# Optimization experiments

Hardware: AMD Instinct MI355X
Metric: run time of the kernel (lower is better)

## Reference

```python
import jax, jax.numpy as jnp
import numpy as np

B, L, F, DM, H, DFF, NL, PRED = 8, 1000, 7, 512, 8, 2048, 4, 50
DK = DM // H           # head dim 64
P = DK // 4            # learned-mask proj dim 16
EPS = 1e-5
SCALE = 1.0 / float(np.sqrt(DK))


def _ln(x, g, b):
    m = jnp.mean(x, -1, keepdims=True)
    v = jnp.mean((x - m) ** 2, -1, keepdims=True)
    return (x - m) / jnp.sqrt(v + EPS) * g + b


def _make_pe():
    pos = np.arange(L, dtype=np.float32)[:, None]
    div = np.exp(np.arange(0, DM, 2, dtype=np.float32) * (-np.log(10000.0) / DM))
    pe = np.zeros((L, DM), dtype=np.float32)
    pe[:, 0::2] = np.sin(pos * div)
    pe[:, 1::2] = np.cos(pos * div)
    return jnp.asarray(pe)


def setup_inputs() -> dict:
    key = jax.random.key(0)
    ks = iter(jax.random.split(key, 40))
    def w(shape, s=0.02):
        return jax.random.normal(next(ks), shape, jnp.float32) * s
    return {
        "x": jax.random.normal(next(ks), (B, L, F), jnp.float32),
        "emb_w": w((F, DM)), "emb_b": jnp.zeros((DM,), jnp.float32),
        "pe": _make_pe(),
        "Wq": w((NL, DM, DM)), "bq": jnp.zeros((NL, DM), jnp.float32),
        "Wk": w((NL, DM, DM)), "bk": jnp.zeros((NL, DM), jnp.float32),
        "Wv": w((NL, DM, DM)), "bv": jnp.zeros((NL, DM), jnp.float32),
        "Wo": w((NL, DM, DM)), "bo": jnp.zeros((NL, DM), jnp.float32),
        "W1": w((NL, DM, DFF)), "b1": jnp.zeros((NL, DFF), jnp.float32),
        "W2": w((NL, DFF, DM)), "b2": jnp.zeros((NL, DM), jnp.float32),
        "g1": jnp.ones((NL, DM), jnp.float32), "be1": jnp.zeros((NL, DM), jnp.float32),
        "g2": jnp.ones((NL, DM), jnp.float32), "be2": jnp.zeros((NL, DM), jnp.float32),
        "lm_qw": w((DK, P)), "lm_qb": jnp.zeros((P,), jnp.float32),
        "lm_kw": w((DK, P)), "lm_kb": jnp.zeros((P,), jnp.float32),
        "gn": jnp.ones((DM,), jnp.float32), "bn": jnp.zeros((DM,), jnp.float32),
        "fc_w": w((DM, PRED)), "fc_b": jnp.zeros((PRED,), jnp.float32),
    }


def reference(x, emb_w, emb_b, pe, Wq, bq, Wk, bk, Wv, bv, Wo, bo,
              W1, b1, W2, b2, g1, be1, g2, be2,
              lm_qw, lm_qb, lm_kw, lm_kb, gn, bn, fc_w, fc_b):
    # eval mode: dropout = identity
    h = x @ emb_w + emb_b + pe[None]                 # [B,L,DM]
    for i in range(NL):
        q = (h @ Wq[i] + bq[i]).reshape(B, L, H, DK)
        k = (h @ Wk[i] + bk[i]).reshape(B, L, H, DK)
        v = (h @ Wv[i] + bv[i]).reshape(B, L, H, DK)
        scores = jnp.einsum('blhd,bshd->bhls', q, k) * SCALE
        # shared LearnedMask: per-head Q/K projection to P dims, tanh bias
        qp = q @ lm_qw + lm_qb                       # [B,L,H,P]
        kp = k @ lm_kw + lm_kb                       # [B,S,H,P]
        scores = scores + jnp.tanh(jnp.einsum('blhp,bshp->bhls', qp, kp))
        attn = jax.nn.softmax(scores, axis=-1)       # mask_flag=False: no mask
        ctx = jnp.einsum('bhls,bshd->blhd', attn, v).reshape(B, L, DM)
        h = _ln(h + ctx @ Wo[i] + bo[i], g1[i], be1[i])
        y = jax.nn.relu(h @ W1[i] + b1[i]) @ W2[i] + b2[i]
        h2 = _ln(h + y, g2[i], be2[i])
        h = _ln(h2 + y, g2[i], be2[i])               # module applies norm2 twice
    h = _ln(h, gn, bn)                               # Encoder final norm
    return h[:, -1, :] @ fc_w + fc_b                 # [B, PRED]
```

## Files before the change

kernel.cpp:

```cpp
#include <hip/hip_runtime.h>
#include <math.h>

#define B_    8
#define L_    1000
#define F_    7
#define DM_   512
#define H_    8
#define DFF_  2048
#define NL_   4
#define PRED_ 50
#define DK_   64
#define P_    16
#define EPS_  1e-5f
#define QKVS  1792

#define L2E_   1.4426950408889634f
#define C_QS   0.18033688011112042f
#define BS_QP  2.8853900817779268f
#define SHFT_  24.0f

typedef unsigned short u16;
typedef __bf16 bf16x8 __attribute__((ext_vector_type(8)));
typedef float  f32x4  __attribute__((ext_vector_type(4)));

__device__ inline float wave_reduce_sum(float x) {
#pragma unroll
  for (int off = 32; off >= 1; off >>= 1) x += __shfl_xor(x, off, 64);
  return x;
}
__device__ inline u16 f2bf(float f) {
  unsigned int u = __float_as_uint(f);
  unsigned int r = u + 0x7FFFu + ((u >> 16) & 1u);
  return (u16)(r >> 16);
}
__device__ inline unsigned int pack2(float a, float b) {
  return (unsigned int)f2bf(a) | ((unsigned int)f2bf(b) << 16);
}
__device__ inline float bf2f(u16 u) { return __uint_as_float(((unsigned int)u) << 16); }
__device__ inline float fexp2(float x) { return __builtin_amdgcn_exp2f(x); }
__device__ inline float frcp(float x) { return __builtin_amdgcn_rcpf(x); }

union bfrag { bf16x8 b; uint4 q; u16 u[8]; };

__device__ inline void gload16(const u16* g, u16* l) {
  __builtin_amdgcn_global_load_lds(
      (const __attribute__((address_space(1))) void*)g,
      (__attribute__((address_space(3))) void*)l, 16, 0, 0);
}

__global__ __launch_bounds__(256)
void transpose_w(const float* __restrict__ in, u16* __restrict__ out,
                 int K, int N, size_t in_lstride, size_t out_lstride,
                 int row_off, int out_ld) {
  __shared__ float tile[32][33];
  int z = blockIdx.z;
  int kk0 = blockIdx.y * 32, nn0 = blockIdx.x * 32;
  int tx = threadIdx.x & 31, ty = threadIdx.x >> 5;
  const float* ip = in + z * in_lstride;
  u16* op = out + z * out_lstride;
#pragma unroll
  for (int i = 0; i < 4; i++)
    tile[ty + i * 8][tx] = ip[(size_t)(kk0 + ty + i * 8) * N + nn0 + tx];
  __syncthreads();
#pragma unroll
  for (int i = 0; i < 4; i++)
    op[(size_t)(row_off + nn0 + ty + i * 8) * out_ld + kk0 + tx] = f2bf(tile[tx][ty + i * 8]);
}

__global__ __launch_bounds__(256)
void wfuse_kernel(const float* __restrict__ Wq, const float* __restrict__ Wk,
                  const float* __restrict__ lmqw, const float* __restrict__ lmkw,
                  u16* __restrict__ Wt) {
  int hh = blockIdx.x, side = blockIdx.y, layer = blockIdx.z;
  const float* W = (side ? Wk : Wq) + (size_t)layer * 512 * 512;
  const float* lw = side ? lmkw : lmqw;
  float scale = side ? 1.0f : BS_QP;
  __shared__ float lws[64][17];
  int t = threadIdx.x;
  for (int i = t; i < 1024; i += 256) lws[i >> 4][i & 15] = lw[i];
  __syncthreads();
  int p = t & 15, kk = t >> 4;
  u16* orow = Wt + (size_t)layer * QKVS * 512 + (size_t)(1536 + side * 128 + hh * 16 + p) * 512;
  for (int kb = 0; kb < 32; kb++) {
    int k = kb * 16 + kk;
    const float* wr = W + (size_t)k * 512 + hh * 64;
    float acc = 0.f;
#pragma unroll
    for (int d = 0; d < 64; d++) acc = fmaf(wr[d], lws[d][p], acc);
    orow[k] = f2bf(acc * scale);
  }
}

__global__ __launch_bounds__(256)
void concat_bias(const float* __restrict__ bq, const float* __restrict__ bk,
                 const float* __restrict__ bv,
                 const float* __restrict__ lmqw, const float* __restrict__ lmqb,
                 const float* __restrict__ lmkw, const float* __restrict__ lmkb,
                 float* __restrict__ bqkv) {
  int i = blockIdx.x * 256 + threadIdx.x;
  int l = i / QKVS, j = i % QKVS;
  float v;
  if (j < 512) v = bq[l * 512 + j];
  else if (j < 1024) v = bk[l * 512 + j - 512];
  else if (j < 1536) v = bv[l * 512 + j - 1024];
  else if (j < 1664) {
    int hh = (j - 1536) >> 4, p = (j - 1536) & 15;
    float acc = lmqb[p];
#pragma unroll
    for (int d = 0; d < 64; d++) acc = fmaf(bq[l * 512 + hh * 64 + d], lmqw[d * 16 + p], acc);
    v = acc * BS_QP;
  } else {
    int hh = (j - 1664) >> 4, p = (j - 1664) & 15;
    float acc = lmkb[p];
#pragma unroll
    for (int d = 0; d < 64; d++) acc = fmaf(bk[l * 512 + hh * 64 + d], lmkw[d * 16 + p], acc);
    v = acc;
  }
  bqkv[i] = v;
}

__global__ __launch_bounds__(512)
void embed_kernel(const float* __restrict__ x, const float* __restrict__ emb_w,
                  const float* __restrict__ emb_b, const float* __restrict__ pe,
                  u16* __restrict__ h16) {
  int bl = blockIdx.x;
  int l = bl % L_;
  int d = threadIdx.x;
  const float* xr = x + (size_t)bl * F_;
  float acc = emb_b[d] + pe[(size_t)l * DM_ + d];
#pragma unroll
  for (int f = 0; f < F_; f++) acc = fmaf(xr[f], emb_w[f * DM_ + d], acc);
  h16[(size_t)bl * DM_ + d] = f2bf(acc);
}

template<int BN>
__global__ __launch_bounds__(256)
void gemm64(const u16* __restrict__ A, const u16* __restrict__ Bt,
            const float* __restrict__ bias, const u16* __restrict__ resid,
            u16* __restrict__ C16, u16* __restrict__ vtg,
            int M, int K, int N, int relu, int nscale, float sval) {
  constexpr int NTW = BN / 32;
  constexpr int BG  = BN / 64;
  constexpr int ASZ = 32 * 64;
  constexpr int BSZ = (BN / 2) * 64;
  __shared__ u16 As[2 * ASZ];
  __shared__ u16 Bs[2 * BSZ];
  int t = threadIdx.x;
  int w = t >> 6, lane = t & 63;
  int wr = w >> 1, wc = w & 1;
  int mloc = lane & 15, quad = lane >> 4;
  int m0 = blockIdx.y * 64, n0 = blockIdx.x * BN;

  const u16* agp; u16* alds;
  {
    int R = w * 8 + (lane >> 3);
    int c = (lane & 7) ^ (R & 7);
    int gm = m0 + 2 * R + (c >> 2); if (gm > M - 1) gm = M - 1;
    agp = A + (size_t)gm * K + (c & 3) * 8;
    alds = As + (w * 8) * 64;
  }
  const u16* bgp[BG]; u16* blds[BG];
#pragma unroll
  for (int j = 0; j < BG; j++) {
    int R = w * (8 * BG) + j * 8 + (lane >> 3);
    int c = (lane & 7) ^ (R & 7);
    bgp[j] = Bt + (size_t)(n0 + 2 * R + (c >> 2)) * K + (c & 3) * 8;
    blds[j] = Bs + (w * (8 * BG) + j * 8) * 64;
  }
  const u16* apt[2];
#pragma unroll
  for (int mi = 0; mi < 2; mi++) {
    int tr = wr * 32 + mi * 16 + mloc;
    int R = tr >> 1, c = (tr & 1) * 4 + quad;
    apt[mi] = As + R * 64 + ((c ^ (R & 7)) * 8);
  }
  const u16* bpt[NTW];
#pragma unroll
  for (int nt = 0; nt < NTW; nt++) {
    int tr = wc * (BN / 2) + nt * 16 + mloc;
    int R = tr >> 1, c = (tr & 1) * 4 + quad;
    bpt[nt] = Bs + R * 64 + ((c ^ (R & 7)) * 8);
  }

  f32x4 acc[2][NTW];
#pragma unroll
  for (int mi = 0; mi < 2; mi++)
#pragma unroll
    for (int nt = 0; nt < NTW; nt++) acc[mi][nt] = (f32x4){0.f, 0.f, 0.f, 0.f};

  gload16(agp, alds);
#pragma unroll
  for (int j = 0; j < BG; j++) gload16(bgp[j], blds[j]);
  __syncthreads();

  const int nk = K >> 5;
  int cur = 0;
  for (int tt = 0; tt < nk; ++tt) {
    if (tt + 1 < nk) {
      const int nxt = cur ^ 1;
      const int koff = (tt + 1) * 32;
      gload16(agp + koff, alds + nxt * ASZ);
#pragma unroll
      for (int j = 0; j < BG; j++) gload16(bgp[j] + koff, blds[j] + nxt * BSZ);
    }
    const int ao = cur * ASZ, bo = cur * BSZ;
    bf16x8 af[2], bv[NTW];
#pragma unroll
    for (int mi = 0; mi < 2; mi++) af[mi] = *(const bf16x8*)(apt[mi] + ao);
#pragma unroll
    for (int nt = 0; nt < NTW; nt++) bv[nt] = *(const bf16x8*)(bpt[nt] + bo);
#pragma unroll
    for (int mi = 0; mi < 2; mi++)
#pragma unroll
      for (int nt = 0; nt < NTW; nt++)
        acc[mi][nt] = __builtin_amdgcn_mfma_f32_16x16x32_bf16(af[mi], bv[nt], acc[mi][nt], 0, 0, 0);
    if (tt + 1 < nk) __syncthreads();
    cur ^= 1;
  }

#pragma unroll
  for (int mi = 0; mi < 2; mi++) {
    int m_r0 = m0 + wr * 32 + mi * 16 + quad * 4;
#pragma unroll
    for (int nt = 0; nt < NTW; nt++) {
      int nbase = n0 + wc * (BN / 2) + nt * 16;
      int n = nbase + mloc;
      if (vtg && nbase >= 1024 && nbase < 1536) {
        if (m_r0 < M) {
          int bb = (m_r0 * 67109) >> 26;
          int ll = m_r0 - bb * 1000;
          int hh2 = (n - 1024) >> 6, dk = n & 63;
          float bn_ = bias[n];
          union { uint2 d; u16 s[4]; } pk;
#pragma unroll
          for (int r = 0; r < 4; r++) pk.s[r] = f2bf(acc[mi][nt][r] + bn_);
          u16* dst = vtg + ((size_t)(bb * 8 + hh2) * 64 + dk) * 1024 + ll;
          *(uint2*)dst = pk.d;
        }
      } else {
        float bn_ = bias[n];
#pragma unroll
        for (int r = 0; r < 4; r++) {
          int m = m_r0 + r;
          if (m >= M) continue;
          size_t crow = (size_t)m * N;
          float vsum = acc[mi][nt][r] + bn_;
          if (resid) vsum += bf2f(resid[crow + n]);
          if (n < nscale) vsum *= sval;
          if (relu) vsum = fmaxf(vsum, 0.f);
          C16[crow + n] = f2bf(vsum);
        }
      }
    }
  }
}

#define KT   64
#define KPLD 24
#define PSLD 40
__global__ __launch_bounds__(256)
void attn_mfma_kernel(const u16* __restrict__ qkv, const u16* __restrict__ vtg,
                      u16* __restrict__ ctx) {
  __shared__ u16 Ks[KT * 64];
  __shared__ u16 Vt[64 * KT];
  __shared__ u16 Kp[KT * KPLD];
  __shared__ u16 Ps[4 * 16 * PSLD];

  int Lid = blockIdx.x;
  int qt = Lid >> 6;
  int bh = ((Lid & 7) << 3) | ((Lid >> 3) & 7);
  int b = bh >> 3, hh = bh & 7;
  int l0 = qt * 64;
  int t = threadIdx.x;
  int wv = t >> 6, lane = t & 63;
  int m = lane & 15, quad = lane >> 4;

  int lq = l0 + wv * 16 + m; if (lq > L_ - 1) lq = L_ - 1;
  const u16* qrow = qkv + (size_t)(b * L_ + lq) * QKVS + hh * DK_;
  bf16x8 qa0 = *(const bf16x8*)(qrow + quad * 8);
  bf16x8 qa1 = *(const bf16x8*)(qrow + 32 + quad * 8);
  bfrag qpa;
  if (quad < 2) {
    qpa.q = *(const uint4*)(qkv + (size_t)(b * L_ + lq) * QKVS + 1536 + hh * P_ + quad * 8);
  } else {
    qpa.q = make_uint4(0u, 0u, 0u, 0u);
  }

  const u16* ks_g = qkv + ((size_t)b * L_ + (t >> 3)) * QKVS + 512 + hh * DK_
                    + ((t & 7) ^ ((t >> 3) & 7)) * 8;
  u16* ks_l = Ks + (t >> 6) * 512;
  const u16* vt_g = vtg + ((size_t)bh * DK_ + (t >> 3)) * 1024
                    + ((t & 7) ^ ((t >> 3) & 7)) * 8;
  u16* vt_l = Vt + (t >> 6) * 512;

  f32x4 O[4];
#pragma unroll
  for (int nt = 0; nt < 4; nt++) O[nt] = (f32x4){0.f, 0.f, 0.f, 0.f};
  float lrun[4] = {0.f, 0.f, 0.f, 0.f};

  u16* pw = Ps + wv * (16 * PSLD);
  const u16* pr0 = pw + m * PSLD + quad * 8;
  const f32x4 zz = (f32x4){0.f, 0.f, 0.f, 0.f};

  for (int s0 = 0; s0 < L_; s0 += KT) {
    uint4 p0, p1;
    if (t < KT) {
      int sg2 = s0 + t; if (sg2 > L_ - 1) sg2 = L_ - 1;
      const u16* pr = qkv + (size_t)(b * L_ + sg2) * QKVS + 1664 + hh * P_;
      p0 = *(const uint4*)(pr);
      p1 = *(const uint4*)(pr + 8);
    }
    __syncthreads();
#pragma unroll
    for (int j = 0; j < 2; j++) {
      gload16(ks_g + ((size_t)s0 + j * 32) * QKVS, ks_l + j * 2048);
      gload16(vt_g + s0 + (size_t)j * 32 * 1024, vt_l + j * 2048);
    }
    if (t < KT) {
      *(uint4*)&Kp[t * KPLD]     = p0;
      *(uint4*)&Kp[t * KPLD + 8] = p1;
    }
    __syncthreads();

#pragma unroll
    for (int kc = 0; kc < 2; kc++) {
      float pv2[2][4];
#pragma unroll
      for (int h2 = 0; h2 < 2; h2++) {
        int nt = kc * 2 + h2;
        const u16* kb = Ks + (nt * 16 + m) * 64;
        int x0 = ((quad) ^ (m & 7)) * 8;
        int x1 = ((4 + quad) ^ (m & 7)) * 8;
        __builtin_amdgcn_s_setprio(1);
        f32x4 sacc = __builtin_amdgcn_mfma_f32_16x16x32_bf16(qa0, *(const bf16x8*)(kb + x0), zz, 0, 0, 0);
        sacc = __builtin_amdgcn_mfma_f32_16x16x32_bf16(qa1, *(const bf16x8*)(kb + x1), sacc, 0, 0, 0);
        bf16x8 kpf = *(const bf16x8*)(Kp + (nt * 16 + m) * KPLD + (quad & 1) * 8);
        f32x4 macc = __builtin_amdgcn_mfma_f32_16x16x32_bf16(qpa.b, kpf, zz, 0, 0, 0);
        __builtin_amdgcn_s_setprio(0);
        bool oob = (s0 + nt * 16 + m) >= L_;
#pragma unroll
        for (int r = 0; r < 4; r++) {
          float e = fexp2(macc[r]);
          float d = frcp(e + 1.f);
          float th = fmaf(d, -2.f * L2E_, L2E_);
          float s = sacc[r] + th;
          if (oob) s = -3e38f;
          float p = fexp2(s - SHFT_);
          pv2[h2][r] = p;
          lrun[r] += p;
        }
      }
#pragma unroll
      for (int h2 = 0; h2 < 2; h2++)
#pragma unroll
        for (int r = 0; r < 4; r++)
          pw[(quad * 4 + r) * PSLD + h2 * 16 + m] = f2bf(pv2[h2][r]);
      bf16x8 pa = *(const bf16x8*)pr0;
      __builtin_amdgcn_s_setprio(1);
#pragma unroll
      for (int ntd = 0; ntd < 4; ntd++) {
        const u16* vb = Vt + (ntd * 16 + m) * KT + (((kc * 4 + quad) ^ (m & 7)) * 8);
        O[ntd] = __builtin_amdgcn_mfma_f32_16x16x32_bf16(pa, *(const bf16x8*)vb, O[ntd], 0, 0, 0);
      }
      __builtin_amdgcn_s_setprio(0);
    }
  }

  float inv[4];
#pragma unroll
  for (int r = 0; r < 4; r++) {
#pragma unroll
    for (int msk = 1; msk < 16; msk <<= 1) lrun[r] += __shfl_xor(lrun[r], msk, 64);
    inv[r] = frcp(lrun[r]);
  }
#pragma unroll
  for (int r = 0; r < 4; r++) {
    int l = l0 + wv * 16 + quad * 4 + r;
    if (l >= L_) continue;
    u16* crow = ctx + ((size_t)(b * L_ + l)) * DM_ + hh * DK_;
#pragma unroll
    for (int nt = 0; nt < 4; nt++) crow[nt * 16 + m] = f2bf(O[nt][r] * inv[r]);
  }
}

__global__ __launch_bounds__(256)
void ln_kernel(const u16* __restrict__ a, const float* __restrict__ g,
               const float* __restrict__ be, u16* __restrict__ o) {
  int wv = threadIdx.x >> 6, lane = threadIdx.x & 63;
  int row = blockIdx.x * 4 + wv;
  size_t base = (size_t)row * DM_ + lane * 8;
  bfrag v; v.q = *(const uint4*)(a + base);
  float x[8], s = 0.f, ss = 0.f;
#pragma unroll
  for (int i = 0; i < 8; i++) { x[i] = bf2f(v.u[i]); s += x[i]; ss = fmaf(x[i], x[i], ss); }
#pragma unroll
  for (int off = 32; off >= 1; off >>= 1) { s += __shfl_xor(s, off, 64); ss += __shfl_xor(ss, off, 64); }
  float mean = s * (1.0f / DM_);
  float var = ss * (1.0f / DM_) - mean * mean;
  float rstd = rsqrtf(var + EPS_);
  float4 g0 = *(const float4*)(g + lane * 8), g1 = *(const float4*)(g + lane * 8 + 4);
  float4 b0 = *(const float4*)(be + lane * 8), b1 = *(const float4*)(be + lane * 8 + 4);
  float gv[8] = {g0.x, g0.y, g0.z, g0.w, g1.x, g1.y, g1.z, g1.w};
  float bv[8] = {b0.x, b0.y, b0.z, b0.w, b1.x, b1.y, b1.z, b1.w};
  bfrag r;
#pragma unroll
  for (int i = 0; i < 8; i++) r.u[i] = f2bf((x[i] - mean) * rstd * gv[i] + bv[i]);
  *(uint4*)(o + base) = r.q;
}

__global__ __launch_bounds__(256)
void ln2x_kernel(const u16* __restrict__ hin, const u16* __restrict__ y,
                 const float* __restrict__ g, const float* __restrict__ be,
                 u16* __restrict__ o16) {
  int wv = threadIdx.x >> 6, lane = threadIdx.x & 63;
  int row = blockIdx.x * 4 + wv;
  size_t base = (size_t)row * DM_ + lane * 8;
  bfrag hv; hv.q = *(const uint4*)(hin + base);
  bfrag yv; yv.q = *(const uint4*)(y + base);
  float4 g0 = *(const float4*)(g + lane * 8), g1 = *(const float4*)(g + lane * 8 + 4);
  float4 b0 = *(const float4*)(be + lane * 8), b1 = *(const float4*)(be + lane * 8 + 4);
  float gv[8] = {g0.x, g0.y, g0.z, g0.w, g1.x, g1.y, g1.z, g1.w};
  float bv[8] = {b0.x, b0.y, b0.z, b0.w, b1.x, b1.y, b1.z, b1.w};
  float x[8], yy[8], s = 0.f, ss = 0.f;
#pragma unroll
  for (int i = 0; i < 8; i++) {
    yy[i] = bf2f(yv.u[i]);
    x[i] = bf2f(hv.u[i]) + yy[i];
    s += x[i]; ss = fmaf(x[i], x[i], ss);
  }
#pragma unroll
  for (int off = 32; off >= 1; off >>= 1) { s += __shfl_xor(s, off, 64); ss += __shfl_xor(ss, off, 64); }
  float mean = s * (1.0f / DM_);
  float var = ss * (1.0f / DM_) - mean * mean;
  float rstd = rsqrtf(var + EPS_);
  float h2[8]; s = 0.f; ss = 0.f;
#pragma unroll
  for (int i = 0; i < 8; i++) {
    h2[i] = (x[i] - mean) * rstd * gv[i] + bv[i] + yy[i];
    s += h2[i]; ss = fmaf(h2[i], h2[i], ss);
  }
#pragma unroll
  for (int off = 32; off >= 1; off >>= 1) { s += __shfl_xor(s, off, 64); ss += __shfl_xor(ss, off, 64); }
  mean = s * (1.0f / DM_);
  var = ss * (1.0f / DM_) - mean * mean;
  rstd = rsqrtf(var + EPS_);
  bfrag r;
#pragma unroll
  for (int i = 0; i < 8; i++) r.u[i] = f2bf((h2[i] - mean) * rstd * gv[i] + bv[i]);
  *(uint4*)(o16 + base) = r.q;
}

__global__ __launch_bounds__(512)
void final_kernel(const u16* __restrict__ h, const float* __restrict__ gn,
                  const float* __restrict__ bn, const float* __restrict__ fcw,
                  const float* __restrict__ fcb, float* __restrict__ out) {
  int b = blockIdx.x;
  int t = threadIdx.x;
  size_t base = ((size_t)b * L_ + (L_ - 1)) * DM_;
  float x = bf2f(h[base + t]);
  float s = wave_reduce_sum(x);
  float ss = wave_reduce_sum(x * x);
  __shared__ float sh_s[8], sh_ss[8];
  int wv = t >> 6, lane = t & 63;
  if (lane == 0) { sh_s[wv] = s; sh_ss[wv] = ss; }
  __syncthreads();
  float S = 0.f, SS = 0.f;
#pragma unroll
  for (int i = 0; i < 8; i++) { S += sh_s[i]; SS += sh_ss[i]; }
  float mean = S * (1.0f / DM_);
  float var = SS * (1.0f / DM_) - mean * mean;
  float rstd = rsqrtf(var + EPS_);
  __shared__ float hn[DM_];
  hn[t] = (x - mean) * rstd * gn[t] + bn[t];
  __syncthreads();
  if (t < PRED_) {
    float acc = fcb[t];
#pragma unroll 8
    for (int d = 0; d < DM_; d++) acc = fmaf(hn[d], fcw[d * PRED_ + t], acc);
    out[b * PRED_ + t] = acc;
  }
}

extern "C" void kernel_launch(void* const* d_in, const int* in_sizes, int n_in,
                              void* d_out, int out_size, void* d_ws, size_t ws_size,
                              hipStream_t stream) {
  const float* x     = (const float*)d_in[0];
  const float* emb_w = (const float*)d_in[1];
  const float* emb_b = (const float*)d_in[2];
  const float* pe    = (const float*)d_in[3];
  const float* Wq = (const float*)d_in[4];  const float* bq = (const float*)d_in[5];
  const float* Wk = (const float*)d_in[6];  const float* bk = (const float*)d_in[7];
  const float* Wv = (const float*)d_in[8];  const float* bv = (const float*)d_in[9];
  const float* Wo = (const float*)d_in[10]; const float* bo = (const float*)d_in[11];
  const float* W1 = (const float*)d_in[12]; const float* b1 = (const float*)d_in[13];
  const float* W2 = (const float*)d_in[14]; const float* b2 = (const float*)d_in[15];
  const float* g1 = (const float*)d_in[16]; const float* be1 = (const float*)d_in[17];
  const float* g2 = (const float*)d_in[18]; const float* be2 = (const float*)d_in[19];
  const float* lm_qw = (const float*)d_in[20]; const float* lm_qb = (const float*)d_in[21];
  const float* lm_kw = (const float*)d_in[22]; const float* lm_kb = (const float*)d_in[23];
  const float* gn = (const float*)d_in[24]; const float* bn = (const float*)d_in[25];
  const float* fc_w = (const float*)d_in[26]; const float* fc_b = (const float*)d_in[27];
  float* out = (float*)d_out;

  const size_t ROWS = (size_t)B_ * L_;
  u16* qkv16 = (u16*)d_ws;
  u16* ctx16 = qkv16 + ROWS * QKVS;
  u16* ffn1  = qkv16;
  u16* h16   = ctx16 + ROWS * DM_;
  u16* t16   = h16 + ROWS * DM_;
  u16* vtg   = t16 + ROWS * DM_;
  u16* Wqkv_t = vtg + (size_t)64 * 64 * 1024;
  u16* Wo_t   = Wqkv_t + (size_t)NL_ * QKVS * DM_;
  u16* W1_t   = Wo_t + (size_t)NL_ * DM_ * DM_;
  u16* W2_t   = W1_t + (size_t)NL_ * DFF_ * DM_;
  float* bqkv = (float*)(W2_t + (size_t)NL_ * DM_ * DFF_);

  transpose_w<<<dim3(16, 16, NL_), 256, 0, stream>>>(Wq, Wqkv_t, DM_, DM_, (size_t)DM_ * DM_, (size_t)QKVS * DM_, 0, DM_);
  transpose_w<<<dim3(16, 16, NL_), 256, 0, stream>>>(Wk, Wqkv_t, DM_, DM_, (size_t)DM_ * DM_, (size_t)QKVS * DM_, 512, DM_);
  transpose_w<<<dim3(16, 16, NL_), 256, 0, stream>>>(Wv, Wqkv_t, DM_, DM_, (size_t)DM_ * DM_, (size_t)QKVS * DM_, 1024, DM_);
  transpose_w<<<dim3(16, 16, NL_), 256, 0, stream>>>(Wo, Wo_t, DM_, DM_, (size_t)DM_ * DM_, (size_t)DM_ * DM_, 0, DM_);
  transpose_w<<<dim3(64, 16, NL_), 256, 0, stream>>>(W1, W1_t, DM_, DFF_, (size_t)DM_ * DFF_, (size_t)DFF_ * DM_, 0, DM_);
  transpose_w<<<dim3(16, 64, NL_), 256, 0, stream>>>(W2, W2_t, DFF_, DM_, (size_t)DFF_ * DM_, (size_t)DM_ * DFF_, 0, DFF_);
  wfuse_kernel<<<dim3(H_, 2, NL_), 256, 0, stream>>>(Wq, Wk, lm_qw, lm_kw, Wqkv_t);
  concat_bias<<<NL_ * QKVS / 256, 256, 0, stream>>>(bq, bk, bv, lm_qw, lm_qb, lm_kw, lm_kb, bqkv);

  embed_kernel<<<dim3((unsigned)ROWS), 512, 0, stream>>>(x, emb_w, emb_b, pe, h16);

  dim3 g_qkv(QKVS / 128, 125);
  dim3 g_ffn1(DFF_ / 128, 125);
  dim3 g_n512(DM_ / 64, 125);
  dim3 g_attn(1024);
  dim3 g_ln(2000);

  for (int i = 0; i < NL_; i++) {
    gemm64<128><<<g_qkv, 256, 0, stream>>>(h16, Wqkv_t + (size_t)i * QKVS * DM_,
        bqkv + i * QKVS, nullptr, qkv16, vtg, 8000, DM_, QKVS, 0, 512, C_QS);

    attn_mfma_kernel<<<g_attn, 256, 0, stream>>>(qkv16, vtg, ctx16);

    gemm64<64><<<g_n512, 256, 0, stream>>>(ctx16, Wo_t + (size_t)i * DM_ * DM_,
        bo + i * DM_, h16, t16, nullptr, 8000, DM_, DM_, 0, 0, 1.0f);
    ln_kernel<<<g_ln, 256, 0, stream>>>(t16, g1 + i * DM_, be1 + i * DM_, h16);

    gemm64<128><<<g_ffn1, 256, 0, stream>>>(h16, W1_t + (size_t)i * DFF_ * DM_,
        b1 + i * DFF_, nullptr, ffn1, nullptr, 8000, DM_, DFF_, 1, 0, 1.0f);
    gemm64<64><<<g_n512, 256, 0, stream>>>(ffn1, W2_t + (size_t)i * DM_ * DFF_,
        b2 + i * DM_, nullptr, t16, nullptr, 8000, DFF_, DM_, 0, 0, 1.0f);

    ln2x_kernel<<<g_ln, 256, 0, stream>>>(h16, t16, g2 + i * DM_, be2 + i * DM_, h16);
  }

  final_kernel<<<B_, 512, 0, stream>>>(h16, gn, bn, fc_w, fc_b, out);
}
```

Measured before the change: 1.033 ms.

## Double-buffer K/V tiles in attention and load key mask projections into registers

The attention kernel now keeps two LDS buffers for the K and V tiles. The next tile's global-to-LDS loads are issued before the current tile's MFMA work, which cuts the loop from two barriers per tile to one and overlaps memory latency with compute. The learned-mask key projection no longer goes through an LDS staging array; each lane reads its fragment straight from global memory into registers. The cost is double the LDS use for K/V, which may lower occupancy, plus unclamped tail reads of the key projection that rely on the out-of-range positions being masked.

Measured after the change: 1.042 ms. No clear change (+0.9%).

```diff
diff --git a/kernel.cpp b/kernel.cpp
--- a/kernel.cpp
+++ b/kernel.cpp
@@ -256,14 +256,12 @@
 }
 
 #define KT   64
-#define KPLD 24
 #define PSLD 40
 __global__ __launch_bounds__(256)
 void attn_mfma_kernel(const u16* __restrict__ qkv, const u16* __restrict__ vtg,
                       u16* __restrict__ ctx) {
-  __shared__ u16 Ks[KT * 64];
-  __shared__ u16 Vt[64 * KT];
-  __shared__ u16 Kp[KT * KPLD];
+  __shared__ u16 Ks[2 * KT * 64];
+  __shared__ u16 Vt[2 * 64 * KT];
   __shared__ u16 Ps[4 * 16 * PSLD];
 
   int Lid = blockIdx.x;
@@ -288,10 +286,11 @@
 
   const u16* ks_g = qkv + ((size_t)b * L_ + (t >> 3)) * QKVS + 512 + hh * DK_
                     + ((t & 7) ^ ((t >> 3) & 7)) * 8;
-  u16* ks_l = Ks + (t >> 6) * 512;
+  u16* ks_l = Ks + wv * 512;
   const u16* vt_g = vtg + ((size_t)bh * DK_ + (t >> 3)) * 1024
                     + ((t & 7) ^ ((t >> 3) & 7)) * 8;
-  u16* vt_l = Vt + (t >> 6) * 512;
+  u16* vt_l = Vt + wv * 512;
+  const u16* kp_g = qkv + (size_t)(b * L_) * QKVS + 1664 + hh * P_ + (quad & 1) * 8;
 
   f32x4 O[4];
 #pragma unroll
@@ -302,25 +301,31 @@
   const u16* pr0 = pw + m * PSLD + quad * 8;
   const f32x4 zz = (f32x4){0.f, 0.f, 0.f, 0.f};
 
-  for (int s0 = 0; s0 < L_; s0 += KT) {
-    uint4 p0, p1;
-    if (t < KT) {
-      int sg2 = s0 + t; if (sg2 > L_ - 1) sg2 = L_ - 1;
-      const u16* pr = qkv + (size_t)(b * L_ + sg2) * QKVS + 1664 + hh * P_;
-      p0 = *(const uint4*)(pr);
-      p1 = *(const uint4*)(pr + 8);
+#pragma unroll
+  for (int j = 0; j < 2; j++) {
+    gload16(ks_g + (size_t)(j * 32) * QKVS, ks_l + j * 2048);
+    gload16(vt_g + (size_t)j * 32 * 1024, vt_l + j * 2048);
+  }
+  __syncthreads();
+
+  for (int tt = 0; tt < 16; ++tt) {
+    const int s0 = tt * KT;
+    const int c = tt & 1;
+    if (tt < 15) {
+      const int sn = s0 + KT, nb = c ^ 1;
+#pragma unroll
+      for (int j = 0; j < 2; j++) {
+        gload16(ks_g + ((size_t)sn + j * 32) * QKVS, ks_l + nb * 4096 + j * 2048);
+        gload16(vt_g + sn + (size_t)j * 32 * 1024, vt_l + nb * 4096 + j * 2048);
+      }
     }
-    __syncthreads();
-#pragma unroll
-    for (int j = 0; j < 2; j++) {
-      gload16(ks_g + ((size_t)s0 + j * 32) * QKVS, ks_l + j * 2048);
-      gload16(vt_g + s0 + (size_t)j * 32 * 1024, vt_l + j * 2048);
-    }
-    if (t < KT) {
-      *(uint4*)&Kp[t * KPLD]     = p0;
-      *(uint4*)&Kp[t * KPLD + 8] = p1;
-    }
-    __syncthreads();
+    bfrag kpr[4];
+#pragma unroll
+    for (int nt = 0; nt < 4; nt++)
+      kpr[nt].q = *(const uint4*)(kp_g + (size_t)(s0 + nt * 16 + m) * QKVS);
+
+    const u16* Kc = Ks + c * 4096;
+    const u16* Vc = Vt + c * 4096;
 
 #pragma unroll
     for (int kc = 0; kc < 2; kc++) {
@@ -328,14 +333,13 @@
 #pragma unroll
       for (int h2 = 0; h2 < 2; h2++) {
         int nt = kc * 2 + h2;
-        const u16* kb = Ks + (nt * 16 + m) * 64;
+        const u16* kb = Kc + (nt * 16 + m) * 64;
         int x0 = ((quad) ^ (m & 7)) * 8;
         int x1 = ((4 + quad) ^ (m & 7)) * 8;
         __builtin_amdgcn_s_setprio(1);
         f32x4 sacc = __builtin_amdgcn_mfma_f32_16x16x32_bf16(qa0, *(const bf16x8*)(kb + x0), zz, 0, 0, 0);
         sacc = __builtin_amdgcn_mfma_f32_16x16x32_bf16(qa1, *(const bf16x8*)(kb + x1), sacc, 0, 0, 0);
-        bf16x8 kpf = *(const bf16x8*)(Kp + (nt * 16 + m) * KPLD + (quad & 1) * 8);
-        f32x4 macc = __builtin_amdgcn_mfma_f32_16x16x32_bf16(qpa.b, kpf, zz, 0, 0, 0);
+        f32x4 macc = __builtin_amdgcn_mfma_f32_16x16x32_bf16(qpa.b, kpr[nt].b, zz, 0, 0, 0);
         __builtin_amdgcn_s_setprio(0);
         bool oob = (s0 + nt * 16 + m) >= L_;
 #pragma unroll
@@ -359,11 +363,12 @@
       __builtin_amdgcn_s_setprio(1);
 #pragma unroll
       for (int ntd = 0; ntd < 4; ntd++) {
-        const u16* vb = Vt + (ntd * 16 + m) * KT + (((kc * 4 + quad) ^ (m & 7)) * 8);
+        const u16* vb = Vc + (ntd * 16 + m) * KT + (((kc * 4 + quad) ^ (m & 7)) * 8);
         O[ntd] = __builtin_amdgcn_mfma_f32_16x16x32_bf16(pa, *(const bf16x8*)vb, O[ntd], 0, 0, 0);
       }
       __builtin_amdgcn_s_setprio(0);
     }
+    if (tt < 15) __syncthreads();
   }
 
   float inv[4];
```
